# Kernel optimization log

Measured on AMD Instinct MI355X. Metric: run time of the kernel, lower is better.

## Reference

```python
import jax, jax.numpy as jnp
import numpy as np

D_MODEL = 1024      # h
KERNEL_DIM = 64
NUM_SCALES = 7      # 1 + ceil(log2(l_max / kernel_dim))
CHANNELS = 1
B = 8
L = 4096            # sequence length == l_max


def _interp_linear(k, scale):
    """torch F.interpolate(mode='linear', align_corners=False) on last axis."""
    if scale == 1:
        return k
    Lin = k.shape[-1]
    Lout = Lin * scale
    coords = (jnp.arange(Lout, dtype=k.dtype) + 0.5) / scale - 0.5
    coords = jnp.clip(coords, 0.0, Lin - 1)
    lo = jnp.floor(coords).astype(jnp.int32)
    hi = jnp.minimum(lo + 1, Lin - 1)
    w = (coords - lo.astype(k.dtype))
    return k[..., lo] * (1.0 - w) + k[..., hi] * w


def setup_inputs() -> dict:
    key = jax.random.key(0)
    ks = jax.random.split(key, NUM_SCALES + 4)
    inp = {"u": jax.random.normal(ks[0], (B, D_MODEL, L), jnp.float32)}
    for i in range(NUM_SCALES):
        inp[f"k{i}"] = jax.random.normal(ks[1 + i], (CHANNELS, D_MODEL, KERNEL_DIM), jnp.float32)
    inp["D"] = jax.random.normal(ks[NUM_SCALES + 1], (CHANNELS, D_MODEL), jnp.float32)
    bound = 1.0 / np.sqrt(CHANNELS * D_MODEL)
    inp["W"] = jax.random.uniform(ks[NUM_SCALES + 2], (D_MODEL, CHANNELS * D_MODEL), jnp.float32, -bound, bound)
    inp["b"] = jax.random.uniform(ks[NUM_SCALES + 3], (D_MODEL,), jnp.float32, -bound, bound)
    return inp


def _gconv(u, kernels, D, W, b):
    # ---- assemble multiscale kernel ('cat' mode, multiplier buffer == 1.0) ----
    parts = [_interp_linear(kernels[i], 2 ** max(0, i - 1)) for i in range(NUM_SCALES)]
    k = jnp.concatenate(parts, axis=-1)                 # (C, H, l_max)
    # kernel_norm buffer is computed detached on first forward
    knorm = jax.lax.stop_gradient(jnp.linalg.norm(k, axis=-1, keepdims=True))
    Lk = k.shape[-1]
    if Lk > L:
        k = k[..., :L]
    elif Lk < L:
        k = jnp.pad(k, ((0, 0), (0, 0), (0, L - Lk)))
    k = k / knorm
    # ---- FFT long convolution (causal, via zero-pad to 2L) ----
    n = 2 * L
    k_f = jnp.fft.rfft(k, n=n)                          # (C, H, n//2+1)
    u_f = jnp.fft.rfft(u, n=n)                          # (B, H, n//2+1)
    y = jnp.fft.irfft(u_f[:, None] * k_f[None], n=n)[..., :L]   # (B, C, H, L)
    # ---- D (skip) term ----
    y = y + u[:, None] * D[None, :, :, None]            # bhl,ch->bchl
    y = y.reshape(y.shape[0], CHANNELS * D_MODEL, L)    # (B, C*H, L)
    # ---- activation (exact GELU), dropout=0, norm=Identity ----
    y = jax.nn.gelu(y, approximate=False)
    # ---- TransposedLinear output projection ----
    y = jnp.einsum('bul,vu->bvl', y, W) + b[None, :, None]
    return y


def reference(u, k0, k1, k2, k3, k4, k5, k6, D, W, b):
    return _gconv(u, [k0, k1, k2, k3, k4, k5, k6], D, W, b)
```

## Files before the change

kernel.cpp:

```cpp
#include <hip/hip_runtime.h>
#include <cstdint>


#define TWO_PI 6.283185307179586f

typedef __bf16 bf16;
typedef __bf16 bf16x4 __attribute__((ext_vector_type(4)));
typedef __bf16 bf16x8 __attribute__((ext_vector_type(8)));
typedef float  f32x4  __attribute__((ext_vector_type(4)));

__device__ __forceinline__ float2 cadd(float2 a, float2 b){ return make_float2(a.x+b.x, a.y+b.y); }
__device__ __forceinline__ float2 csub(float2 a, float2 b){ return make_float2(a.x-b.x, a.y-b.y); }
__device__ __forceinline__ float2 cmul(float2 a, float2 b){ return make_float2(a.x*b.x-a.y*b.y, a.x*b.y+a.y*b.x); }

template<int SIGN>
__device__ __forceinline__ float2 rot90(float2 c) {
  return (SIGN < 0) ? make_float2(c.y, -c.x) : make_float2(-c.y, c.x);
}

template<int SIGN>
__device__ __forceinline__ void dft16(float2 v[16])
{
  const float C1 = 0.92387953251128675613f;
  const float S1 = 0.38268343236508977173f;
  const float SQ = 0.70710678118654752440f;
  const float sg = (SIGN < 0) ? -1.0f : 1.0f;
  const float2 w16[10] = {
    make_float2(1.f, 0.f),        make_float2(C1,  sg*S1),
    make_float2(SQ,  sg*SQ),      make_float2(S1,  sg*C1),
    make_float2(0.f, sg*1.f),     make_float2(-S1, sg*C1),
    make_float2(-SQ, sg*SQ),      make_float2(-C1, sg*S1),
    make_float2(-1.f, 0.f),       make_float2(-C1, -sg*S1)
  };
  float2 w[16];
  #pragma unroll
  for (int s0 = 0; s0 < 4; ++s0) {
    float2 a0 = v[s0], a1 = v[s0+4], a2 = v[s0+8], a3 = v[s0+12];
    float2 t0 = cadd(a0,a2), t1 = csub(a0,a2);
    float2 t2 = cadd(a1,a3);
    float2 j3 = rot90<SIGN>(csub(a1,a3));
    w[s0+0]  = cadd(t0,t2);
    w[s0+4]  = cadd(t1,j3);
    w[s0+8]  = csub(t0,t2);
    w[s0+12] = csub(t1,j3);
  }
  #pragma unroll
  for (int s0 = 1; s0 < 4; ++s0)
    #pragma unroll
    for (int f0 = 1; f0 < 4; ++f0)
      w[s0+4*f0] = cmul(w[s0+4*f0], w16[s0*f0]);
  #pragma unroll
  for (int f0 = 0; f0 < 4; ++f0) {
    float2 a0 = w[4*f0], a1 = w[1+4*f0], a2 = w[2+4*f0], a3 = w[3+4*f0];
    float2 t0 = cadd(a0,a2), t1 = csub(a0,a2);
    float2 t2 = cadd(a1,a3);
    float2 j3 = rot90<SIGN>(csub(a1,a3));
    v[f0+0]  = cadd(t0,t2);
    v[f0+4]  = cadd(t1,j3);
    v[f0+8]  = csub(t0,t2);
    v[f0+12] = csub(t1,j3);
  }
}

__device__ __forceinline__ void twiddle15(float2 v[16], float ang)
{
  float sn, cs; __sincosf(ang, &sn, &cs);
  float2 w1 = make_float2(cs, sn);
  float2 cur = w1;
  v[1] = cmul(v[1], cur);
  #pragma unroll
  for (int f = 2; f < 16; ++f) { cur = cmul(cur, w1); v[f] = cmul(v[f], cur); }
}

#define LDSP(n) ((n) + ((n) >> 4))

template<int SIGN>
__device__ inline void fft4096(float2* bufA, float2* bufB, int tid)
{
  float2* src = bufA;
  float2* dst = bufB;
  #pragma unroll
  for (int s = 0; s < 6; ++s) {
    const int m = 1 << (2*s);
    __syncthreads();
    #pragma unroll
    for (int it = 0; it < 4; ++it) {
      int bid = tid + it*256;
      int k = bid & (m-1);
      int j = bid >> (2*s);
      int rbase = k + m*j;
      float2 c0 = src[rbase];
      float2 c1 = src[rbase + 1024];
      float2 c2 = src[rbase + 2048];
      float2 c3 = src[rbase + 3072];
      float2 t0 = cadd(c0, c2);
      float2 t1 = csub(c0, c2);
      float2 t2 = cadd(c1, c3);
      float2 dd = csub(c1, c3);
      float2 t3 = (SIGN < 0) ? make_float2(dd.y, -dd.x) : make_float2(-dd.y, dd.x);
      float ang = (float)SIGN * (TWO_PI/4096.0f) * (float)(j << (2*s));
      float sn, cs;
      __sincosf(ang, &sn, &cs);
      float2 w1 = make_float2(cs, sn);
      float2 w2 = cmul(w1, w1);
      float2 w3 = cmul(w2, w1);
      int wbase = k + 4*m*j;
      dst[wbase]       = cadd(t0, t2);
      dst[wbase + m]   = cmul(w1, cadd(t1, t3));
      dst[wbase + 2*m] = cmul(w2, csub(t0, t2));
      dst[wbase + 3*m] = cmul(w3, csub(t1, t3));
    }
    float2* tmp = src; src = dst; dst = tmp;
  }
  __syncthreads();
}

__global__ __launch_bounds__(256) void prep_kf_kernel(
    const float* __restrict__ k0, const float* __restrict__ k1, const float* __restrict__ k2,
    const float* __restrict__ k3, const float* __restrict__ k4, const float* __restrict__ k5,
    const float* __restrict__ k6, float2* __restrict__ Kf)
{
  extern __shared__ __align__(16) float2 smem[];
  float2* bufA = smem;
  float2* bufB = smem + 4096;
  float*  kk   = (float*)bufB;
  float*  red  = (float*)bufA;
  int tid = threadIdx.x;
  int d = blockIdx.x;
  const float* kp[7] = { k0 + d*64, k1 + d*64, k2 + d*64, k3 + d*64,
                         k4 + d*64, k5 + d*64, k6 + d*64 };
  #pragma unroll
  for (int it = 0; it < 16; ++it) {
    int idx = tid + it*256;
    int seg, s, base;
    if      (idx <   64) { seg=0; s=1;  base=0;    }
    else if (idx <  128) { seg=1; s=1;  base=64;   }
    else if (idx <  256) { seg=2; s=2;  base=128;  }
    else if (idx <  512) { seg=3; s=4;  base=256;  }
    else if (idx < 1024) { seg=4; s=8;  base=512;  }
    else if (idx < 2048) { seg=5; s=16; base=1024; }
    else                 { seg=6; s=32; base=2048; }
    int j = idx - base;
    float coord = ((float)j + 0.5f) / (float)s - 0.5f;
    coord = fminf(fmaxf(coord, 0.0f), 63.0f);
    int lo = (int)coord;
    int hi = min(lo + 1, 63);
    float w = coord - (float)lo;
    const float* kpp = kp[seg];
    kk[idx] = kpp[lo] * (1.0f - w) + kpp[hi] * w;
  }
  __syncthreads();
  float psum = 0.f;
  #pragma unroll
  for (int it = 0; it < 16; ++it) { float v = kk[tid + it*256]; psum += v*v; }
  red[tid] = psum;
  __syncthreads();
  if (tid == 0) {
    float tot = 0.f;
    for (int i = 0; i < 256; ++i) tot += red[i];
    red[0] = 1.0f / sqrtf(tot);
  }
  __syncthreads();
  float inv = red[0];
  __syncthreads();
  #pragma unroll
  for (int it = 0; it < 8; ++it) {
    int m_ = tid + it*256;
    bufA[m_]        = make_float2(kk[2*m_] * inv, kk[2*m_+1] * inv);
    bufA[m_ + 2048] = make_float2(0.f, 0.f);
  }
  fft4096<-1>(bufA, bufB, tid);
  const float S = 1.0f/4096.0f;
  float2* kfr = Kf + (size_t)d * 4104;
  for (int j = tid; j < 2048; j += 256) {
    if (j == 0) {
      float2 Z0 = bufA[0];
      kfr[0]    = make_float2((Z0.x + Z0.y) * S, 0.f);
      kfr[4096] = make_float2((Z0.x - Z0.y) * S, 0.f);
      float2 Zh = bufA[2048];
      kfr[2048] = make_float2(Zh.x * S, -Zh.y * S);
    } else {
      float2 Zj = bufA[j];
      float2 Zm = bufA[4096 - j];
      float2 E = make_float2(0.5f*(Zj.x + Zm.x), 0.5f*(Zj.y - Zm.y));
      float2 O = make_float2(0.5f*(Zj.y + Zm.y), 0.5f*(Zm.x - Zj.x));
      float ang = -(TWO_PI/8192.0f) * (float)j;
      float sn, cs; __sincosf(ang, &sn, &cs);
      float2 W = make_float2(cs, sn);
      float2 T = cmul(W, O);
      kfr[j]        = make_float2((E.x + T.x)*S, (E.y + T.y)*S);
      kfr[4096 - j] = make_float2((E.x - T.x)*S, (T.y - E.y)*S);
    }
  }
}

__global__ __launch_bounds__(256) void wcast_kernel(const float* __restrict__ W,
                                                    bf16* __restrict__ Wbf)
{
  int i4 = blockIdx.x * 256 + threadIdx.x;
  float4 v = ((const float4*)W)[i4];
  bf16x4 h; h[0] = (bf16)v.x; h[1] = (bf16)v.y; h[2] = (bf16)v.z; h[3] = (bf16)v.w;
  *(bf16x4*)(Wbf + (size_t)i4 * 4) = h;
}

__global__ __launch_bounds__(256, 4) void fftconv_kernel(
    const float* __restrict__ u, const float* __restrict__ Dv,
    const float2* __restrict__ Kf, bf16* __restrict__ ynat)
{
  __shared__ __align__(16) float2 lds[4352];
  int tid = threadIdx.x;
  int d = blockIdx.x >> 3;
  int b = blockIdx.x & 7;
  int row = b * 1024 + d;
  const float* uRow = u + (size_t)row * 4096;
  const float2* uR2 = (const float2*)uRow;
  const float4* uR4 = (const float4*)uRow;

  float2 v[16];
  int f1g = tid >> 4;
  int lo4 = tid & 15;

  #pragma unroll
  for (int s = 0; s < 8; ++s)  v[s] = uR2[tid + 256*s];
  #pragma unroll
  for (int s = 8; s < 16; ++s) v[s] = make_float2(0.f, 0.f);
  dft16<-1>(v);
  twiddle15(v, -(TWO_PI/4096.0f) * (float)tid);
  {
    int base = tid + (tid >> 4);
    #pragma unroll
    for (int f = 0; f < 16; ++f) lds[f*272 + base] = v[f];
  }
  __syncthreads();
  #pragma unroll
  for (int t1 = 0; t1 < 16; ++t1) v[t1] = lds[f1g*272 + lo4 + 17*t1];
  __syncthreads();
  dft16<-1>(v);
  twiddle15(v, -(TWO_PI/256.0f) * (float)lo4);
  #pragma unroll
  for (int f = 0; f < 16; ++f) lds[f1g*272 + lo4*17 + f] = v[f];
  __syncthreads();
  #pragma unroll
  for (int t0 = 0; t0 < 16; ++t0) v[t0] = lds[f1g*272 + t0*17 + lo4];
  __syncthreads();
  dft16<-1>(v);
  #pragma unroll
  for (int k3 = 0; k3 < 16; ++k3) lds[f1g + 17*lo4 + 272*k3] = v[k3];
  __syncthreads();

  const float2* kfr = Kf + (size_t)d * 4104;
  #pragma unroll
  for (int it = 0; it < 8; ++it) {
    int j = tid + it*256;
    if (j == 0) {
      float2 Z0 = lds[LDSP(0)];
      float X0 = Z0.x + Z0.y;
      float XM = Z0.x - Z0.y;
      float P0 = X0 * kfr[0].x;
      float PM = XM * kfr[4096].x;
      lds[LDSP(0)] = make_float2(0.5f*(P0 + PM), 0.5f*(P0 - PM));
      float2 Zh = lds[LDSP(2048)];
      float2 Xh = make_float2(Zh.x, -Zh.y);
      float2 Ph = cmul(Xh, kfr[2048]);
      lds[LDSP(2048)] = make_float2(Ph.x, -Ph.y);
    } else {
      float2 Zj = lds[LDSP(j)];
      float2 Zm = lds[LDSP(4096 - j)];
      float2 E = make_float2(0.5f*(Zj.x + Zm.x), 0.5f*(Zj.y - Zm.y));
      float2 O = make_float2(0.5f*(Zj.y + Zm.y), 0.5f*(Zm.x - Zj.x));
      float ang = -(TWO_PI/8192.0f) * (float)j;
      float sn, cs; __sincosf(ang, &sn, &cs);
      float2 W = make_float2(cs, sn);
      float2 T = cmul(W, O);
      float2 Xj = cadd(E, T);
      float2 Xm = make_float2(E.x - T.x, T.y - E.y);
      float2 Pj = cmul(Xj, kfr[j]);
      float2 Pm = cmul(Xm, kfr[4096 - j]);
      float2 Ep = make_float2(0.5f*(Pj.x + Pm.x), 0.5f*(Pj.y - Pm.y));
      float2 V  = make_float2(0.5f*(Pj.x - Pm.x), 0.5f*(Pj.y + Pm.y));
      float2 Wi = make_float2(cs, -sn);
      float2 Op = cmul(Wi, V);
      lds[LDSP(j)]        = make_float2(Ep.x - Op.y, Ep.y + Op.x);
      lds[LDSP(4096 - j)] = make_float2(Ep.x + Op.y, Op.x - Ep.y);
    }
  }
  __syncthreads();

  {
    int base = tid + (tid >> 4);
    #pragma unroll
    for (int s = 0; s < 16; ++s) v[s] = lds[base + 272*s];
    __syncthreads();
    dft16<1>(v);
    twiddle15(v, (TWO_PI/4096.0f) * (float)tid);
    #pragma unroll
    for (int f = 0; f < 16; ++f) lds[f*272 + base] = v[f];
  }
  __syncthreads();
  #pragma unroll
  for (int t1 = 0; t1 < 16; ++t1) v[t1] = lds[f1g*272 + lo4 + 17*t1];
  __syncthreads();
  dft16<1>(v);
  twiddle15(v, (TWO_PI/256.0f) * (float)lo4);
  #pragma unroll
  for (int f = 0; f < 16; ++f) lds[f1g*272 + lo4*17 + f] = v[f];
  __syncthreads();
  #pragma unroll
  for (int t0 = 0; t0 < 16; ++t0) v[t0] = lds[f1g*272 + t0*17 + lo4];
  __syncthreads();
  dft16<1>(v);
  #pragma unroll
  for (int k3 = 0; k3 < 16; ++k3) lds[f1g + 17*lo4 + 272*k3] = v[k3];
  __syncthreads();

  float Dd = Dv[d];
  float vals[16];
  int base = 8*tid + (tid >> 1);
  #pragma unroll
  for (int i = 0; i < 8; ++i) {
    float2 q = lds[base + i];
    vals[2*i]   = q.x;
    vals[2*i+1] = q.y;
  }
  #pragma unroll
  for (int c = 0; c < 4; ++c) {
    float4 uu = uR4[tid*4 + c];
    vals[4*c+0] += uu.x * Dd;
    vals[4*c+1] += uu.y * Dd;
    vals[4*c+2] += uu.z * Dd;
    vals[4*c+3] += uu.w * Dd;
  }
  union { bf16 h[16]; uint4 q[2]; } st;
  #pragma unroll
  for (int i = 0; i < 16; ++i) {
    float x = vals[i];
    float g = 0.5f * x * (1.0f + erff(x * 0.70710678118654752440f));
    st.h[i] = (bf16)g;
  }
  uint4* outp = (uint4*)(ynat + (size_t)row * 4096 + tid * 16);
  outp[0] = st.q[0];
  outp[1] = st.q[1];
}

__global__ __launch_bounds__(256) void transpose_kernel(const ushort* __restrict__ ynat,
                                                        ushort* __restrict__ yT)
{
  __shared__ ushort T[64 * 68];
  int tid = threadIdx.x;
  int l0 = blockIdx.x * 64;
  int u0 = blockIdx.y * 64;
  int b  = blockIdx.z;
  const ushort* src = ynat + ((size_t)(b*1024 + u0)) * 4096 + l0;
  #pragma unroll
  for (int it = 0; it < 4; ++it) {
    int c = tid + it*256;
    int r = c >> 4;
    int c4 = c & 15;
    ushort4 v = *(const ushort4*)(src + (size_t)r * 4096 + c4*4);
    *(ushort4*)&T[r*68 + c4*4] = v;
  }
  __syncthreads();
  ushort* dst = yT + ((size_t)(b*4096 + l0)) * 1024 + u0;
  #pragma unroll
  for (int it = 0; it < 4; ++it) {
    int c = tid + it*256;
    int lr = c >> 4;
    int u4 = c & 15;
    ushort4 v;
    v.x = T[(u4*4+0)*68 + lr];
    v.y = T[(u4*4+1)*68 + lr];
    v.z = T[(u4*4+2)*68 + lr];
    v.w = T[(u4*4+3)*68 + lr];
    *(ushort4*)(dst + (size_t)lr * 1024 + u4*4) = v;
  }
}

#define GL_LDS16(g, l) __builtin_amdgcn_global_load_lds( \
    (const __attribute__((address_space(1))) void*)(g),  \
    (__attribute__((address_space(3))) void*)(l), 16, 0, 0)

__global__ __launch_bounds__(256) void gemm_kernel(
    const bf16* __restrict__ A,
    const bf16* __restrict__ B,
    const float* __restrict__ bias,
    float* __restrict__ out)
{
  __shared__ bf16 ldsA[128 * 32];
  __shared__ bf16 ldsB[128 * 32];
  int tid = threadIdx.x;
  int lane = tid & 63;
  int w = tid >> 6;
  int wm = w & 1, wn = w >> 1;
  int m0 = blockIdx.x * 128;
  int n0 = blockIdx.y * 128;
  int lrow = lane & 15;
  int quad = lane >> 4;
  f32x4 acc[4][4] = {};
  for (int kk0 = 0; kk0 < 1024; kk0 += 32) {
    __syncthreads();
    #pragma unroll
    for (int i = 0; i < 2; ++i) {
      int c = tid + 256*i;
      int row = c >> 2;
      int kc = c & 3;
      const bf16* ga = A + (size_t)(m0 + row) * 1024 + kk0 + kc*8;
      bf16* la = ldsA + (size_t)(w*64 + 256*i) * 8;
      GL_LDS16(ga, la);
      const bf16* gb = B + (size_t)(n0 + row) * 1024 + kk0 + kc*8;
      bf16* lb = ldsB + (size_t)(w*64 + 256*i) * 8;
      GL_LDS16(gb, lb);
    }
    __syncthreads();
    bf16x8 a[4], bq[4];
    #pragma unroll
    for (int mi = 0; mi < 4; ++mi)
      a[mi] = *(const bf16x8*)&ldsA[(wm*64 + mi*16 + lrow)*32 + quad*8];
    #pragma unroll
    for (int ni = 0; ni < 4; ++ni)
      bq[ni] = *(const bf16x8*)&ldsB[(wn*64 + ni*16 + lrow)*32 + quad*8];
    #pragma unroll
    for (int mi = 0; mi < 4; ++mi)
      #pragma unroll
      for (int ni = 0; ni < 4; ++ni)
        acc[mi][ni] = __builtin_amdgcn_mfma_f32_16x16x32_bf16(a[mi], bq[ni], acc[mi][ni], 0, 0, 0);
  }
  #pragma unroll
  for (int mi = 0; mi < 4; ++mi) {
    #pragma unroll
    for (int r = 0; r < 4; ++r) {
      int vrow = m0 + wm*64 + mi*16 + quad*4 + r;
      float bv = bias[vrow];
      #pragma unroll
      for (int ni = 0; ni < 4; ++ni) {
        int n = n0 + wn*64 + ni*16 + lrow;
        int bidx = n >> 12;
        int l = n & 4095;
        out[((size_t)bidx << 22) + ((size_t)vrow << 12) + l] = acc[mi][ni][r] + bv;
      }
    }
  }
}

extern "C" void kernel_launch(void* const* d_in, const int* in_sizes, int n_in,
                              void* d_out, int out_size, void* d_ws, size_t ws_size,
                              hipStream_t stream)
{
  const float* u  = (const float*)d_in[0];
  const float* k0 = (const float*)d_in[1];
  const float* k1 = (const float*)d_in[2];
  const float* k2 = (const float*)d_in[3];
  const float* k3 = (const float*)d_in[4];
  const float* k4 = (const float*)d_in[5];
  const float* k5 = (const float*)d_in[6];
  const float* k6 = (const float*)d_in[7];
  const float* Dv = (const float*)d_in[8];
  const float* W  = (const float*)d_in[9];
  const float* bs = (const float*)d_in[10];
  float* out = (float*)d_out;

  char* ws = (char*)d_ws;
  float2* Kf  = (float2*)(ws);
  bf16*  Wbf  = (bf16*)(ws + 33619968);
  bf16*  ynat = (bf16*)(ws + 35717120);
  bf16*  yT   = (bf16*)(ws + 102825984);

  hipLaunchKernelGGL(prep_kf_kernel, dim3(1024), dim3(256), 65536, stream,
                     k0, k1, k2, k3, k4, k5, k6, Kf);
  hipLaunchKernelGGL(wcast_kernel, dim3(1024), dim3(256), 0, stream, W, Wbf);
  hipLaunchKernelGGL(fftconv_kernel, dim3(8192), dim3(256), 0, stream, u, Dv, Kf, ynat);
  hipLaunchKernelGGL(transpose_kernel, dim3(64, 16, 8), dim3(256), 0, stream,
                     (const ushort*)ynat, (ushort*)yT);
  hipLaunchKernelGGL(gemm_kernel, dim3(8, 256), dim3(256), 0, stream, Wbf, yT, bs, out);
}
```

Before: 495.8 us.

## Precompute folded real-FFT spectral coefficients and use tanh GELU approximation

The kernel spectrum is stored as three precomputed coefficient arrays that fold the real-FFT unpack, the pointwise multiply and the repack into a single linear map on the packed complex spectrum. This removes the per-element sincos and most of the butterfly arithmetic from the hot conv kernel, at the cost of reading three coefficient arrays instead of two entries. The exact erf GELU is replaced with the tanh-form approximation using fast exp and reciprocal, which adds small approximation error. The prep-kernel norm reduction now uses wave shuffles, and the workspace is re-laid out so yT aliases the coefficient buffers.

```diff
diff --git a/kernel.cpp b/kernel.cpp
--- a/kernel.cpp
+++ b/kernel.cpp
@@ -118,7 +118,8 @@
 __global__ __launch_bounds__(256) void prep_kf_kernel(
     const float* __restrict__ k0, const float* __restrict__ k1, const float* __restrict__ k2,
     const float* __restrict__ k3, const float* __restrict__ k4, const float* __restrict__ k5,
-    const float* __restrict__ k6, float2* __restrict__ Kf)
+    const float* __restrict__ k6,
+    float2* __restrict__ CFa, float2* __restrict__ CFb, float2* __restrict__ CFd)
 {
   extern __shared__ __align__(16) float2 smem[];
   float2* bufA = smem;
@@ -155,10 +156,11 @@
   for (int it = 0; it < 16; ++it) { float v = kk[tid + it*256]; psum += v*v; }
   red[tid] = psum;
   __syncthreads();
-  if (tid == 0) {
-    float tot = 0.f;
-    for (int i = 0; i < 256; ++i) tot += red[i];
-    red[0] = 1.0f / sqrtf(tot);
+  if (tid < 64) {
+    float s = red[tid] + red[tid+64] + red[tid+128] + red[tid+192];
+    #pragma unroll
+    for (int off = 32; off >= 1; off >>= 1) s += __shfl_xor(s, off, 64);
+    if (tid == 0) red[0] = 1.0f / sqrtf(s);
   }
   __syncthreads();
   float inv = red[0];
@@ -171,14 +173,18 @@
   }
   fft4096<-1>(bufA, bufB, tid);
   const float S = 1.0f/4096.0f;
-  float2* kfr = Kf + (size_t)d * 4104;
+  float2* cfa = CFa + (size_t)d * 2048;
+  float2* cfb = CFb + (size_t)d * 2048;
+  float2* cfd = CFd + (size_t)d * 2048;
   for (int j = tid; j < 2048; j += 256) {
     if (j == 0) {
       float2 Z0 = bufA[0];
-      kfr[0]    = make_float2((Z0.x + Z0.y) * S, 0.f);
-      kfr[4096] = make_float2((Z0.x - Z0.y) * S, 0.f);
+      float K0 = (Z0.x + Z0.y) * S;
+      float KM = (Z0.x - Z0.y) * S;
+      cfa[0] = make_float2(0.5f*(K0 + KM), 0.5f*(K0 - KM));
       float2 Zh = bufA[2048];
-      kfr[2048] = make_float2(Zh.x * S, -Zh.y * S);
+      cfb[0] = make_float2(Zh.x * S, Zh.y * S);
+      cfd[0] = make_float2(0.f, 0.f);
     } else {
       float2 Zj = bufA[j];
       float2 Zm = bufA[4096 - j];
@@ -188,8 +194,17 @@
       float sn, cs; __sincosf(ang, &sn, &cs);
       float2 W = make_float2(cs, sn);
       float2 T = cmul(W, O);
-      kfr[j]        = make_float2((E.x + T.x)*S, (E.y + T.y)*S);
-      kfr[4096 - j] = make_float2((E.x - T.x)*S, (T.y - E.y)*S);
+      float2 Kj  = make_float2((E.x + T.x)*S, (E.y + T.y)*S);
+      float2 Kmc = make_float2((E.x - T.x)*S, (E.y - T.y)*S);
+      float s = -sn;
+      float c = cs;
+      float2 al = make_float2(0.5f*((1.f-s)*Kj.x + (1.f+s)*Kmc.x),
+                              0.5f*((1.f-s)*Kj.y + (1.f+s)*Kmc.y));
+      float2 z = make_float2(Kj.x - Kmc.x, Kj.y - Kmc.y);
+      float2 be = make_float2(-0.5f*c*z.y, 0.5f*c*z.x);
+      float2 de = make_float2( 0.5f*((1.f+s)*Kj.x + (1.f-s)*Kmc.x),
+                              -0.5f*((1.f+s)*Kj.y + (1.f-s)*Kmc.y));
+      cfa[j] = al; cfb[j] = be; cfd[j] = de;
     }
   }
 }
@@ -205,7 +220,8 @@
 
 __global__ __launch_bounds__(256, 4) void fftconv_kernel(
     const float* __restrict__ u, const float* __restrict__ Dv,
-    const float2* __restrict__ Kf, bf16* __restrict__ ynat)
+    const float2* __restrict__ CFa, const float2* __restrict__ CFb,
+    const float2* __restrict__ CFd, bf16* __restrict__ ynat)
 {
   __shared__ __align__(16) float2 lds[4352];
   int tid = threadIdx.x;
@@ -248,40 +264,32 @@
   for (int k3 = 0; k3 < 16; ++k3) lds[f1g + 17*lo4 + 272*k3] = v[k3];
   __syncthreads();
 
-  const float2* kfr = Kf + (size_t)d * 4104;
+  const float2* cfa = CFa + (size_t)d * 2048;
+  const float2* cfb = CFb + (size_t)d * 2048;
+  const float2* cfd = CFd + (size_t)d * 2048;
   #pragma unroll
   for (int it = 0; it < 8; ++it) {
     int j = tid + it*256;
     if (j == 0) {
+      float2 a0 = cfa[0];
       float2 Z0 = lds[LDSP(0)];
-      float X0 = Z0.x + Z0.y;
-      float XM = Z0.x - Z0.y;
-      float P0 = X0 * kfr[0].x;
-      float PM = XM * kfr[4096].x;
-      lds[LDSP(0)] = make_float2(0.5f*(P0 + PM), 0.5f*(P0 - PM));
+      lds[LDSP(0)] = make_float2(a0.x*Z0.x + a0.y*Z0.y, a0.y*Z0.x + a0.x*Z0.y);
+      float2 b0 = cfb[0];
       float2 Zh = lds[LDSP(2048)];
-      float2 Xh = make_float2(Zh.x, -Zh.y);
-      float2 Ph = cmul(Xh, kfr[2048]);
-      lds[LDSP(2048)] = make_float2(Ph.x, -Ph.y);
+      lds[LDSP(2048)] = cmul(Zh, b0);
     } else {
+      float2 al = cfa[j];
+      float2 be = cfb[j];
+      float2 de = cfd[j];
       float2 Zj = lds[LDSP(j)];
       float2 Zm = lds[LDSP(4096 - j)];
-      float2 E = make_float2(0.5f*(Zj.x + Zm.x), 0.5f*(Zj.y - Zm.y));
-      float2 O = make_float2(0.5f*(Zj.y + Zm.y), 0.5f*(Zm.x - Zj.x));
-      float ang = -(TWO_PI/8192.0f) * (float)j;
-      float sn, cs; __sincosf(ang, &sn, &cs);
-      float2 W = make_float2(cs, sn);
-      float2 T = cmul(W, O);
-      float2 Xj = cadd(E, T);
-      float2 Xm = make_float2(E.x - T.x, T.y - E.y);
-      float2 Pj = cmul(Xj, kfr[j]);
-      float2 Pm = cmul(Xm, kfr[4096 - j]);
-      float2 Ep = make_float2(0.5f*(Pj.x + Pm.x), 0.5f*(Pj.y - Pm.y));
-      float2 V  = make_float2(0.5f*(Pj.x - Pm.x), 0.5f*(Pj.y + Pm.y));
-      float2 Wi = make_float2(cs, -sn);
-      float2 Op = cmul(Wi, V);
-      lds[LDSP(j)]        = make_float2(Ep.x - Op.y, Ep.y + Op.x);
-      lds[LDSP(4096 - j)] = make_float2(Ep.x + Op.y, Op.x - Ep.y);
+      float2 Zmc = make_float2(Zm.x, -Zm.y);
+      float2 Qj = cadd(cmul(al, Zj), cmul(be, Zmc));
+      float2 nbc = make_float2(-be.x, be.y);
+      float2 Zjc = make_float2(Zj.x, -Zj.y);
+      float2 Qm = cadd(cmul(nbc, Zjc), cmul(de, Zm));
+      lds[LDSP(j)]        = Qj;
+      lds[LDSP(4096 - j)] = Qm;
     }
   }
   __syncthreads();
@@ -334,7 +342,10 @@
   #pragma unroll
   for (int i = 0; i < 16; ++i) {
     float x = vals[i];
-    float g = 0.5f * x * (1.0f + erff(x * 0.70710678118654752440f));
+    float x2 = x * x;
+    float q = x * (0.7978845608f + 0.0356774081f * x2);
+    float e = __expf(-2.0f * q);
+    float g = x * __builtin_amdgcn_rcpf(1.0f + e);
     st.h[i] = (bf16)g;
   }
   uint4* outp = (uint4*)(ynat + (size_t)row * 4096 + tid * 16);
@@ -459,15 +470,18 @@
   float* out = (float*)d_out;
 
   char* ws = (char*)d_ws;
-  float2* Kf  = (float2*)(ws);
-  bf16*  Wbf  = (bf16*)(ws + 33619968);
-  bf16*  ynat = (bf16*)(ws + 35717120);
-  bf16*  yT   = (bf16*)(ws + 102825984);
+  float2* CFa = (float2*)(ws);
+  float2* CFb = (float2*)(ws + 16777216);
+  float2* CFd = (float2*)(ws + 33554432);
+  bf16*  yT   = (bf16*)(ws);
+  bf16*  Wbf  = (bf16*)(ws + 67108864);
+  bf16*  ynat = (bf16*)(ws + 69206016);
 
   hipLaunchKernelGGL(prep_kf_kernel, dim3(1024), dim3(256), 65536, stream,
-                     k0, k1, k2, k3, k4, k5, k6, Kf);
+                     k0, k1, k2, k3, k4, k5, k6, CFa, CFb, CFd);
   hipLaunchKernelGGL(wcast_kernel, dim3(1024), dim3(256), 0, stream, W, Wbf);
-  hipLaunchKernelGGL(fftconv_kernel, dim3(8192), dim3(256), 0, stream, u, Dv, Kf, ynat);
+  hipLaunchKernelGGL(fftconv_kernel, dim3(8192), dim3(256), 0, stream,
+                     u, Dv, CFa, CFb, CFd, ynat);
   hipLaunchKernelGGL(transpose_kernel, dim3(64, 16, 8), dim3(256), 0, stream,
                      (const ushort*)ynat, (ushort*)yT);
   hipLaunchKernelGGL(gemm_kernel, dim3(8, 256), dim3(256), 0, stream, Wbf, yT, bs, out);
```

New measurement: 470.3 us. 1.05x faster.
